# Performance work log

Hardware: AMD Instinct MI355X
Metric: run time of the kernel (lower is better)

## Reference

```python
import jax, jax.numpy as jnp
import numpy as np

B = 4096
T = 66            # total_char_ids = 51 + 8 + 6 + 1
EMB = 128
ITEM_EMB = 64     # emb_dim // 2
NUM_ITEMS = 287
ITEMS_IN_GAME = 70  # 7 * 10
N_SCREEN = 24
N_MINI = 40
CONT = 32


def _unique_ids(key, batch, n):
    keys = jax.random.split(key, batch)
    return jax.vmap(lambda k: jax.random.permutation(k, T)[:n])(keys).astype(jnp.int32)


def setup_inputs() -> dict:
    key = jax.random.key(0)
    ks = jax.random.split(key, 16)
    inp = {
        "continuous_f": jax.random.normal(ks[0], (B, CONT), jnp.float32),
        "screen_feats": jax.random.uniform(ks[1], (B, N_SCREEN, 4), jnp.float32),
        "minimap_feats": jax.random.uniform(ks[2], (B, N_MINI, 2), jnp.float32),
        "char_emb": jax.random.normal(ks[3], (T, EMB), jnp.float32) * 0.02,
        "item_emb": jax.random.normal(ks[4], (NUM_ITEMS, ITEM_EMB), jnp.float32) * 0.02,
        "Ws1": jax.random.normal(ks[5], (EMB + 4, EMB), jnp.float32) * 0.05,
        "bs1": jnp.zeros((EMB,), jnp.float32),
        "Ws2": jax.random.normal(ks[6], (EMB, EMB), jnp.float32) * 0.05,
        "bs2": jnp.zeros((EMB,), jnp.float32),
        "Wm1": jax.random.normal(ks[7], (EMB + 2, EMB), jnp.float32) * 0.05,
        "bm1": jnp.zeros((EMB,), jnp.float32),
        "Wm2": jax.random.normal(ks[8], (EMB, EMB), jnp.float32) * 0.05,
        "bm2": jnp.zeros((EMB,), jnp.float32),
        "screen_ids": _unique_ids(ks[9], B, N_SCREEN),
        "minimap_ids": _unique_ids(ks[10], B, N_MINI),
        "items": jax.random.randint(ks[11], (B, ITEMS_IN_GAME), 0, NUM_ITEMS, jnp.int32),
    }
    return inp


def reference(continuous_f, screen_feats, minimap_feats, char_emb, item_emb,
              Ws1, bs1, Ws2, bs2, Wm1, bm1, Wm2, bm2,
              screen_ids, minimap_ids, items):
    b = continuous_f.shape[0]
    rows = jnp.arange(b)[:, None]

    # scatter detections by char id into fixed [T, .] buffers (vectorized over batch)
    scr = jnp.zeros((b, T, 4), screen_feats.dtype).at[rows, screen_ids].set(screen_feats)
    mini = jnp.zeros((b, T, 2), minimap_feats.dtype).at[rows, minimap_ids].set(minimap_feats)

    # item embedding lookup -> [b, 70*64]
    item_flat = item_emb[items].reshape(b, -1)

    base = jnp.broadcast_to(char_emb, (b, T, EMB))  # all char ids embedded

    def mlp(x, W1, b1, W2, b2):
        h = jax.nn.relu(jnp.einsum('btf,fh->bth', x, W1) + b1)
        return jnp.einsum('bth,hk->btk', h, W2) + b2

    screen_out = mlp(jnp.concatenate([base, scr], axis=-1), Ws1, bs1, Ws2, bs2)
    mini_out = mlp(jnp.concatenate([base, mini], axis=-1), Wm1, bm1, Wm2, bm2)

    obs = jnp.concatenate(
        [continuous_f, screen_out.reshape(b, -1), mini_out.reshape(b, -1), item_flat],
        axis=-1)  # [b, 32 + 66*128 + 66*128 + 70*64] = [b, 21408]
    return obs
```

## Files before the change

### kernel.cpp

```cpp
#include <hip/hip_runtime.h>
#include <stdint.h>

#define BDIM 256
#define T_   66
#define EMB  128
#define NS   24
#define NM   40
#define NI   70
#define CONT 32
#define OUTW 21408

typedef __attribute__((ext_vector_type(4))) float f32x4;
typedef __attribute__((ext_vector_type(8))) unsigned short u16x8;
typedef __attribute__((ext_vector_type(8))) __bf16 bf16x8;

static __device__ __forceinline__ unsigned short f2bf(float x) {
  union { float f; unsigned u; } v; v.f = x;
  unsigned r = (v.u + 0x7FFFu + ((v.u >> 16) & 1u)) >> 16;
  return (unsigned short)r;
}

static __device__ __forceinline__ f32x4 mfma16(u16x8 a, u16x8 b, f32x4 c) {
  return __builtin_amdgcn_mfma_f32_16x16x32_bf16(
      __builtin_bit_cast(bf16x8, a), __builtin_bit_cast(bf16x8, b), c, 0, 0, 0);
}

__global__ __launch_bounds__(BDIM) void precomp(
    const float* __restrict__ char_emb,
    const float* __restrict__ Ws1, const float* __restrict__ bs1,
    const float* __restrict__ Ws2, const float* __restrict__ bs2,
    const float* __restrict__ Wm1, const float* __restrict__ bm1,
    const float* __restrict__ Wm2, const float* __restrict__ bm2,
    float* __restrict__ base_h_s, float* __restrict__ base_h_m,
    float* __restrict__ base_out_s, float* __restrict__ base_out_m,
    unsigned short* __restrict__ w2s_swz, unsigned short* __restrict__ w2m_swz) {
  const int bb = blockIdx.x, tid = threadIdx.x;
  if (bb < 132) {
    const int mlp = bb / T_, t = bb % T_;
    const float* W1 = mlp ? Wm1 : Ws1;
    const float* W2 = mlp ? Wm2 : Ws2;
    const float* b1 = mlp ? bm1 : bs1;
    const float* b2 = mlp ? bm2 : bs2;
    float* bh = mlp ? base_h_m : base_h_s;
    float* bo = mlp ? base_out_m : base_out_s;
    __shared__ float h[EMB];
    if (tid < EMB) {
      float acc = b1[tid];
      for (int f = 0; f < EMB; ++f) acc += char_emb[t * EMB + f] * W1[f * EMB + tid];
      bh[t * EMB + tid] = acc;
      h[tid] = fmaxf(acc, 0.f);
    }
    __syncthreads();
    if (tid < EMB) {
      float acc = b2[tid];
      for (int i = 0; i < EMB; ++i) acc += h[i] * W2[i * EMB + tid];
      bo[t * EMB + tid] = acc;
    }
  } else {
    const int mlp = bb - 132;
    const float* W2 = mlp ? Wm2 : Ws2;
    unsigned short* dst = mlp ? w2m_swz : w2s_swz;
    for (int idx = tid; idx < 8 * 4 * 64 * 8; idx += BDIM) {
      const int e = idx & 7, lane = (idx >> 3) & 63, kk = (idx >> 9) & 3, n = idx >> 11;
      const int k = kk * 32 + (lane >> 4) * 8 + e;
      const int col = n * 16 + (lane & 15);
      dst[idx] = f2bf(W2[k * EMB + col]);
    }
  }
}

__global__ __launch_bounds__(BDIM) void fused(
    const float* __restrict__ contf,
    const float* __restrict__ sfeat,
    const float* __restrict__ mfeat,
    const float* __restrict__ item_emb,
    const float* __restrict__ Ws1,
    const float* __restrict__ bs2,
    const float* __restrict__ Wm1,
    const float* __restrict__ bm2,
    const int* __restrict__ sids,
    const int* __restrict__ mids,
    const int* __restrict__ items,
    const float* __restrict__ base_h_s, const float* __restrict__ base_h_m,
    const float* __restrict__ base_out_s, const float* __restrict__ base_out_m,
    const unsigned short* __restrict__ w2s_swz, const unsigned short* __restrict__ w2m_swz,
    float* __restrict__ out) {
  const int b = blockIdx.x, tid = threadIdx.x;

  __shared__ int s_map[T_], m_map[T_];
  __shared__ int s_id[NS], m_id[NM], s_item[NI];
  __shared__ float s_f[NS * 4], m_f[NM * 2];
  __shared__ u16x8 h_frag[5 * 4 * 64];
  __shared__ float det_out[48 * 132];

  if (tid < T_) { s_map[tid] = -1; m_map[tid] = -1; }
  if (tid < NS) s_id[tid] = sids[b * NS + tid];
  if (tid < NM) m_id[tid] = mids[b * NM + tid];
  if (tid < NI) s_item[tid] = items[b * NI + tid];
  if (tid < NS * 4) s_f[tid] = sfeat[b * NS * 4 + tid];
  if (tid < NM * 2) m_f[tid] = mfeat[b * NM * 2 + tid];
  __syncthreads();
  if (tid < NS) s_map[s_id[tid]] = tid;
  if (tid < NM) m_map[m_id[tid]] = tid;

  for (int u = tid; u < 5 * 4 * 64; u += BDIM) {
    const int lane = u & 63, kk = (u >> 6) & 3, tile = u >> 8;
    const int g = lane >> 4, r = lane & 15;
    const int k0 = kk * 32 + g * 8;
    const bool scr = tile < 2;
    const int j = scr ? tile * 16 + r : (tile - 2) * 16 + r;
    const int nd = scr ? NS : NM;
    float v[8];
    if (j < nd) {
      const int t = scr ? s_id[j] : m_id[j];
      const float* bh = (scr ? base_h_s : base_h_m) + t * EMB + k0;
#pragma unroll
      for (int e = 0; e < 8; ++e) v[e] = bh[e];
      if (scr) {
        const float* fp = &s_f[j * 4];
#pragma unroll
        for (int c = 0; c < 4; ++c) {
          const float fc = fp[c];
          const float* w = Ws1 + (128 + c) * EMB + k0;
#pragma unroll
          for (int e = 0; e < 8; ++e) v[e] += fc * w[e];
        }
      } else {
        const float* fp = &m_f[j * 2];
#pragma unroll
        for (int c = 0; c < 2; ++c) {
          const float fc = fp[c];
          const float* w = Wm1 + (128 + c) * EMB + k0;
#pragma unroll
          for (int e = 0; e < 8; ++e) v[e] += fc * w[e];
        }
      }
#pragma unroll
      for (int e = 0; e < 8; ++e) v[e] = fmaxf(v[e], 0.f);
    } else {
#pragma unroll
      for (int e = 0; e < 8; ++e) v[e] = 0.f;
    }
    u16x8 pk;
#pragma unroll
    for (int e = 0; e < 8; ++e) pk[e] = f2bf(v[e]);
    h_frag[u] = pk;
  }
  __syncthreads();

  {
    f32x4* ob = reinterpret_cast<f32x4*>(out + (size_t)b * OUTW);
    const f32x4* cb = reinterpret_cast<const f32x4*>(contf + (size_t)b * CONT);
    for (int u = tid; u < 8 + NI * 16; u += BDIM) {
      if (u < 8) {
        __builtin_nontemporal_store(cb[u], &ob[u]);
      } else {
        const int v2 = u - 8, j = v2 >> 4, q = v2 & 15;
        const int it = s_item[j];
        const f32x4 src = reinterpret_cast<const f32x4*>(item_emb + it * 64)[q];
        __builtin_nontemporal_store(src, reinterpret_cast<f32x4*>(
            out + (size_t)b * OUTW + (CONT + 2 * T_ * EMB) + j * 64) + q);
      }
    }
  }

  const int w = tid >> 6, lane = tid & 63;
  const int g = lane >> 4, r = lane & 15;
  const int n0 = w * 2;

  {
    u16x8 bS[2][4];
    float biasS[2];
#pragma unroll
    for (int n = 0; n < 2; ++n) {
      biasS[n] = bs2[(n0 + n) * 16 + r];
#pragma unroll
      for (int kk = 0; kk < 4; ++kk)
        bS[n][kk] = reinterpret_cast<const u16x8*>(w2s_swz)[((n0 + n) * 4 + kk) * 64 + lane];
    }
#pragma unroll
    for (int m = 0; m < 2; ++m) {
#pragma unroll
      for (int n = 0; n < 2; ++n) {
        f32x4 acc = {0.f, 0.f, 0.f, 0.f};
#pragma unroll
        for (int kk = 0; kk < 4; ++kk)
          acc = mfma16(h_frag[(m * 4 + kk) * 64 + lane], bS[n][kk], acc);
        const int col = (n0 + n) * 16 + r;
#pragma unroll
        for (int q = 0; q < 4; ++q)
          det_out[(m * 16 + g * 4 + q) * 132 + col] = acc[q] + biasS[n];
      }
    }
  }
  __syncthreads();

  {
    float* outp = out + (size_t)b * OUTW + CONT;
    for (int u = tid; u < T_ * 32; u += BDIM) {
      const int t = u >> 5, q = u & 31;
      const int d = s_map[t];
      f32x4 v;
      if (d >= 0) v = *reinterpret_cast<const f32x4*>(&det_out[d * 132 + q * 4]);
      else        v = reinterpret_cast<const f32x4*>(base_out_s + t * EMB)[q];
      __builtin_nontemporal_store(v, reinterpret_cast<f32x4*>(outp + t * EMB) + q);
    }
  }
  __syncthreads();

  {
    u16x8 bM[2][4];
    float biasM[2];
#pragma unroll
    for (int n = 0; n < 2; ++n) {
      biasM[n] = bm2[(n0 + n) * 16 + r];
#pragma unroll
      for (int kk = 0; kk < 4; ++kk)
        bM[n][kk] = reinterpret_cast<const u16x8*>(w2m_swz)[((n0 + n) * 4 + kk) * 64 + lane];
    }
#pragma unroll
    for (int m = 0; m < 3; ++m) {
#pragma unroll
      for (int n = 0; n < 2; ++n) {
        f32x4 acc = {0.f, 0.f, 0.f, 0.f};
#pragma unroll
        for (int kk = 0; kk < 4; ++kk)
          acc = mfma16(h_frag[((m + 2) * 4 + kk) * 64 + lane], bM[n][kk], acc);
        const int col = (n0 + n) * 16 + r;
#pragma unroll
        for (int q = 0; q < 4; ++q)
          det_out[(m * 16 + g * 4 + q) * 132 + col] = acc[q] + biasM[n];
      }
    }
  }
  __syncthreads();

  {
    float* outp = out + (size_t)b * OUTW + CONT + T_ * EMB;
    for (int u = tid; u < T_ * 32; u += BDIM) {
      const int t = u >> 5, q = u & 31;
      const int d = m_map[t];
      f32x4 v;
      if (d >= 0) v = *reinterpret_cast<const f32x4*>(&det_out[d * 132 + q * 4]);
      else        v = reinterpret_cast<const f32x4*>(base_out_m + t * EMB)[q];
      __builtin_nontemporal_store(v, reinterpret_cast<f32x4*>(outp + t * EMB) + q);
    }
  }
}

extern "C" void kernel_launch(void* const* d_in, const int* in_sizes, int n_in,
                              void* d_out, int out_size, void* d_ws, size_t ws_size,
                              hipStream_t stream) {
  const float* contf    = (const float*)d_in[0];
  const float* sfeat    = (const float*)d_in[1];
  const float* mfeat    = (const float*)d_in[2];
  const float* char_emb = (const float*)d_in[3];
  const float* item_emb = (const float*)d_in[4];
  const float* Ws1 = (const float*)d_in[5];
  const float* bs1 = (const float*)d_in[6];
  const float* Ws2 = (const float*)d_in[7];
  const float* bs2 = (const float*)d_in[8];
  const float* Wm1 = (const float*)d_in[9];
  const float* bm1 = (const float*)d_in[10];
  const float* Wm2 = (const float*)d_in[11];
  const float* bm2 = (const float*)d_in[12];
  const int* sids  = (const int*)d_in[13];
  const int* mids  = (const int*)d_in[14];
  const int* items = (const int*)d_in[15];
  float* out = (float*)d_out;

  const int B = in_sizes[0] / CONT;

  char* ws = (char*)d_ws;
  float* base_h_s   = (float*)(ws + 0);
  float* base_h_m   = (float*)(ws + 33792);
  float* base_out_s = (float*)(ws + 67584);
  float* base_out_m = (float*)(ws + 101376);
  unsigned short* w2s = (unsigned short*)(ws + 135168);
  unsigned short* w2m = (unsigned short*)(ws + 167936);

  precomp<<<134, BDIM, 0, stream>>>(char_emb, Ws1, bs1, Ws2, bs2, Wm1, bm1, Wm2, bm2,
                                    base_h_s, base_h_m, base_out_s, base_out_m, w2s, w2m);
  fused<<<B, BDIM, 0, stream>>>(contf, sfeat, mfeat, item_emb, Ws1, bs2, Wm1, bm2,
                                sids, mids, items,
                                base_h_s, base_h_m, base_out_s, base_out_m, w2s, w2m, out);
}
```

Baseline: 98.12 us.

## Scatter MFMA results straight to global, drop LDS staging, widen blocks to 512

The fused kernel now writes each detection's MLP output directly from the MFMA accumulators to its scattered output row, and writes base rows only for char ids with no detection. This removes the det_out LDS buffer and the extra barriers between the screen and minimap phases. Block size doubles to 512 so each wave owns one 16-column N tile, and the bias is folded into the accumulator init. The precompute kernel splits the K dimension across four thread groups and covers both MLPs in one block. The price is scalar scattered global stores, narrower than the previous 16-byte vector writes, and lower occupancy per CU from the larger blocks.

Measured after the change: 99.00 us. About the same (+0.9%).

```diff
diff --git a/kernel.cpp b/kernel.cpp
--- a/kernel.cpp
+++ b/kernel.cpp
@@ -1,7 +1,8 @@
 #include <hip/hip_runtime.h>
 #include <stdint.h>
 
-#define BDIM 256
+#define BDIM 512
+#define PDIM 512
 #define T_   66
 #define EMB  128
 #define NS   24
@@ -25,7 +26,7 @@
       __builtin_bit_cast(bf16x8, a), __builtin_bit_cast(bf16x8, b), c, 0, 0, 0);
 }
 
-__global__ __launch_bounds__(BDIM) void precomp(
+__global__ __launch_bounds__(PDIM) void precomp(
     const float* __restrict__ char_emb,
     const float* __restrict__ Ws1, const float* __restrict__ bs1,
     const float* __restrict__ Ws2, const float* __restrict__ bs2,
@@ -35,32 +36,45 @@
     float* __restrict__ base_out_s, float* __restrict__ base_out_m,
     unsigned short* __restrict__ w2s_swz, unsigned short* __restrict__ w2m_swz) {
   const int bb = blockIdx.x, tid = threadIdx.x;
-  if (bb < 132) {
-    const int mlp = bb / T_, t = bb % T_;
+  if (bb < T_) {
+    const int t = bb;
+    const int quarter = tid >> 7;
+    const int col = tid & 127;
+    const int mlp = quarter & 1;
+    const int kh = quarter >> 1;
     const float* W1 = mlp ? Wm1 : Ws1;
     const float* W2 = mlp ? Wm2 : Ws2;
     const float* b1 = mlp ? bm1 : bs1;
     const float* b2 = mlp ? bm2 : bs2;
     float* bh = mlp ? base_h_m : base_h_s;
     float* bo = mlp ? base_out_m : base_out_s;
-    __shared__ float h[EMB];
-    if (tid < EMB) {
-      float acc = b1[tid];
-      for (int f = 0; f < EMB; ++f) acc += char_emb[t * EMB + f] * W1[f * EMB + tid];
-      bh[t * EMB + tid] = acc;
-      h[tid] = fmaxf(acc, 0.f);
-    }
+    __shared__ float part[4][EMB];
+    __shared__ float h[2][EMB];
+    float acc = 0.f;
+#pragma unroll 8
+    for (int f = kh * 64; f < kh * 64 + 64; ++f)
+      acc += char_emb[t * EMB + f] * W1[f * EMB + col];
+    part[quarter][col] = acc;
     __syncthreads();
-    if (tid < EMB) {
-      float acc = b2[tid];
-      for (int i = 0; i < EMB; ++i) acc += h[i] * W2[i * EMB + tid];
-      bo[t * EMB + tid] = acc;
-    }
+    if (tid < 256) {
+      const float v = b1[col] + part[mlp][col] + part[2 + mlp][col];
+      bh[t * EMB + col] = v;
+      h[mlp][col] = fmaxf(v, 0.f);
+    }
+    __syncthreads();
+    float acc2 = 0.f;
+#pragma unroll 8
+    for (int i = kh * 64; i < kh * 64 + 64; ++i)
+      acc2 += h[mlp][i] * W2[i * EMB + col];
+    part[quarter][col] = acc2;
+    __syncthreads();
+    if (tid < 256)
+      bo[t * EMB + col] = b2[col] + part[mlp][col] + part[2 + mlp][col];
   } else {
-    const int mlp = bb - 132;
+    const int mlp = bb - T_;
     const float* W2 = mlp ? Wm2 : Ws2;
     unsigned short* dst = mlp ? w2m_swz : w2s_swz;
-    for (int idx = tid; idx < 8 * 4 * 64 * 8; idx += BDIM) {
+    for (int idx = tid; idx < 8 * 4 * 64 * 8; idx += PDIM) {
       const int e = idx & 7, lane = (idx >> 3) & 63, kk = (idx >> 9) & 3, n = idx >> 11;
       const int k = kk * 32 + (lane >> 4) * 8 + e;
       const int col = n * 16 + (lane & 15);
@@ -91,7 +105,6 @@
   __shared__ int s_id[NS], m_id[NM], s_item[NI];
   __shared__ float s_f[NS * 4], m_f[NM * 2];
   __shared__ u16x8 h_frag[5 * 4 * 64];
-  __shared__ float det_out[48 * 132];
 
   if (tid < T_) { s_map[tid] = -1; m_map[tid] = -1; }
   if (tid < NS) s_id[tid] = sids[b * NS + tid];
@@ -100,9 +113,9 @@
   if (tid < NS * 4) s_f[tid] = sfeat[b * NS * 4 + tid];
   if (tid < NM * 2) m_f[tid] = mfeat[b * NM * 2 + tid];
   __syncthreads();
+
   if (tid < NS) s_map[s_id[tid]] = tid;
   if (tid < NM) m_map[m_id[tid]] = tid;
-
   for (int u = tid; u < 5 * 4 * 64; u += BDIM) {
     const int lane = u & 63, kk = (u >> 6) & 3, tile = u >> 8;
     const int g = lane >> 4, r = lane & 15;
@@ -121,18 +134,18 @@
 #pragma unroll
         for (int c = 0; c < 4; ++c) {
           const float fc = fp[c];
-          const float* w = Ws1 + (128 + c) * EMB + k0;
-#pragma unroll
-          for (int e = 0; e < 8; ++e) v[e] += fc * w[e];
+          const float* wp = Ws1 + (128 + c) * EMB + k0;
+#pragma unroll
+          for (int e = 0; e < 8; ++e) v[e] += fc * wp[e];
         }
       } else {
         const float* fp = &m_f[j * 2];
 #pragma unroll
         for (int c = 0; c < 2; ++c) {
           const float fc = fp[c];
-          const float* w = Wm1 + (128 + c) * EMB + k0;
-#pragma unroll
-          for (int e = 0; e < 8; ++e) v[e] += fc * w[e];
+          const float* wp = Wm1 + (128 + c) * EMB + k0;
+#pragma unroll
+          for (int e = 0; e < 8; ++e) v[e] += fc * wp[e];
         }
       }
 #pragma unroll
@@ -147,10 +160,72 @@
     h_frag[u] = pk;
   }
   __syncthreads();
+
+  const int lane = tid & 63, w = tid >> 6;
+  const int g = lane >> 4, r = lane & 15;
+  const int n = w;
+  float* outS = out + (size_t)b * OUTW + CONT;
+  float* outM = outS + T_ * EMB;
+
+  u16x8 bS[4], bM[4];
+#pragma unroll
+  for (int kk = 0; kk < 4; ++kk) {
+    bS[kk] = reinterpret_cast<const u16x8*>(w2s_swz)[(n * 4 + kk) * 64 + lane];
+    bM[kk] = reinterpret_cast<const u16x8*>(w2m_swz)[(n * 4 + kk) * 64 + lane];
+  }
+  const float biasS = bs2[n * 16 + r];
+  const float biasM = bm2[n * 16 + r];
+
+#pragma unroll
+  for (int m = 0; m < 2; ++m) {
+    f32x4 acc = {biasS, biasS, biasS, biasS};
+#pragma unroll
+    for (int kk = 0; kk < 4; ++kk)
+      acc = mfma16(h_frag[(m * 4 + kk) * 64 + lane], bS[kk], acc);
+#pragma unroll
+    for (int q = 0; q < 4; ++q) {
+      const int rd = m * 16 + g * 4 + q;
+      if (rd < NS) {
+        const int t = s_id[rd];
+        __builtin_nontemporal_store(acc[q], outS + t * EMB + n * 16 + r);
+      }
+    }
+  }
+#pragma unroll
+  for (int m = 0; m < 3; ++m) {
+    f32x4 acc = {biasM, biasM, biasM, biasM};
+#pragma unroll
+    for (int kk = 0; kk < 4; ++kk)
+      acc = mfma16(h_frag[((m + 2) * 4 + kk) * 64 + lane], bM[kk], acc);
+#pragma unroll
+    for (int q = 0; q < 4; ++q) {
+      const int rd = m * 16 + g * 4 + q;
+      if (rd < NM) {
+        const int t = m_id[rd];
+        __builtin_nontemporal_store(acc[q], outM + t * EMB + n * 16 + r);
+      }
+    }
+  }
+
+  for (int u = tid; u < T_ * 32; u += BDIM) {
+    const int t = u >> 5, q = u & 31;
+    if (s_map[t] < 0) {
+      const f32x4 v = reinterpret_cast<const f32x4*>(base_out_s + t * EMB)[q];
+      __builtin_nontemporal_store(v, reinterpret_cast<f32x4*>(outS + t * EMB) + q);
+    }
+  }
+  for (int u = tid; u < T_ * 32; u += BDIM) {
+    const int t = u >> 5, q = u & 31;
+    if (m_map[t] < 0) {
+      const f32x4 v = reinterpret_cast<const f32x4*>(base_out_m + t * EMB)[q];
+      __builtin_nontemporal_store(v, reinterpret_cast<f32x4*>(outM + t * EMB) + q);
+    }
+  }
 
   {
     f32x4* ob = reinterpret_cast<f32x4*>(out + (size_t)b * OUTW);
     const f32x4* cb = reinterpret_cast<const f32x4*>(contf + (size_t)b * CONT);
+    float* outI = out + (size_t)b * OUTW + (CONT + 2 * T_ * EMB);
     for (int u = tid; u < 8 + NI * 16; u += BDIM) {
       if (u < 8) {
         __builtin_nontemporal_store(cb[u], &ob[u]);
@@ -158,92 +233,8 @@
         const int v2 = u - 8, j = v2 >> 4, q = v2 & 15;
         const int it = s_item[j];
         const f32x4 src = reinterpret_cast<const f32x4*>(item_emb + it * 64)[q];
-        __builtin_nontemporal_store(src, reinterpret_cast<f32x4*>(
-            out + (size_t)b * OUTW + (CONT + 2 * T_ * EMB) + j * 64) + q);
-      }
-    }
-  }
-
-  const int w = tid >> 6, lane = tid & 63;
-  const int g = lane >> 4, r = lane & 15;
-  const int n0 = w * 2;
-
-  {
-    u16x8 bS[2][4];
-    float biasS[2];
-#pragma unroll
-    for (int n = 0; n < 2; ++n) {
-      biasS[n] = bs2[(n0 + n) * 16 + r];
-#pragma unroll
-      for (int kk = 0; kk < 4; ++kk)
-        bS[n][kk] = reinterpret_cast<const u16x8*>(w2s_swz)[((n0 + n) * 4 + kk) * 64 + lane];
-    }
-#pragma unroll
-    for (int m = 0; m < 2; ++m) {
-#pragma unroll
-      for (int n = 0; n < 2; ++n) {
-        f32x4 acc = {0.f, 0.f, 0.f, 0.f};
-#pragma unroll
-        for (int kk = 0; kk < 4; ++kk)
-          acc = mfma16(h_frag[(m * 4 + kk) * 64 + lane], bS[n][kk], acc);
-        const int col = (n0 + n) * 16 + r;
-#pragma unroll
-        for (int q = 0; q < 4; ++q)
-          det_out[(m * 16 + g * 4 + q) * 132 + col] = acc[q] + biasS[n];
-      }
-    }
-  }
-  __syncthreads();
-
-  {
-    float* outp = out + (size_t)b * OUTW + CONT;
-    for (int u = tid; u < T_ * 32; u += BDIM) {
-      const int t = u >> 5, q = u & 31;
-      const int d = s_map[t];
-      f32x4 v;
-      if (d >= 0) v = *reinterpret_cast<const f32x4*>(&det_out[d * 132 + q * 4]);
-      else        v = reinterpret_cast<const f32x4*>(base_out_s + t * EMB)[q];
-      __builtin_nontemporal_store(v, reinterpret_cast<f32x4*>(outp + t * EMB) + q);
-    }
-  }
-  __syncthreads();
-
-  {
-    u16x8 bM[2][4];
-    float biasM[2];
-#pragma unroll
-    for (int n = 0; n < 2; ++n) {
-      biasM[n] = bm2[(n0 + n) * 16 + r];
-#pragma unroll
-      for (int kk = 0; kk < 4; ++kk)
-        bM[n][kk] = reinterpret_cast<const u16x8*>(w2m_swz)[((n0 + n) * 4 + kk) * 64 + lane];
-    }
-#pragma unroll
-    for (int m = 0; m < 3; ++m) {
-#pragma unroll
-      for (int n = 0; n < 2; ++n) {
-        f32x4 acc = {0.f, 0.f, 0.f, 0.f};
-#pragma unroll
-        for (int kk = 0; kk < 4; ++kk)
-          acc = mfma16(h_frag[((m + 2) * 4 + kk) * 64 + lane], bM[n][kk], acc);
-        const int col = (n0 + n) * 16 + r;
-#pragma unroll
-        for (int q = 0; q < 4; ++q)
-          det_out[(m * 16 + g * 4 + q) * 132 + col] = acc[q] + biasM[n];
-      }
-    }
-  }
-  __syncthreads();
-
-  {
-    float* outp = out + (size_t)b * OUTW + CONT + T_ * EMB;
-    for (int u = tid; u < T_ * 32; u += BDIM) {
-      const int t = u >> 5, q = u & 31;
-      const int d = m_map[t];
-      f32x4 v;
-      if (d >= 0) v = *reinterpret_cast<const f32x4*>(&det_out[d * 132 + q * 4]);
-      else        v = reinterpret_cast<const f32x4*>(base_out_m + t * EMB)[q];
-      __builtin_nontemporal_store(v, reinterpret_cast<f32x4*>(outp + t * EMB) + q);
+        __builtin_nontemporal_store(src, reinterpret_cast<f32x4*>(outI + j * 64) + q);
+      }
     }
   }
 }
@@ -279,8 +270,8 @@
   unsigned short* w2s = (unsigned short*)(ws + 135168);
   unsigned short* w2m = (unsigned short*)(ws + 167936);
 
-  precomp<<<134, BDIM, 0, stream>>>(char_emb, Ws1, bs1, Ws2, bs2, Wm1, bm1, Wm2, bm2,
-                                    base_h_s, base_h_m, base_out_s, base_out_m, w2s, w2m);
+  precomp<<<T_ + 2, PDIM, 0, stream>>>(char_emb, Ws1, bs1, Ws2, bs2, Wm1, bm1, Wm2, bm2,
+                                       base_h_s, base_h_m, base_out_s, base_out_m, w2s, w2m);
   fused<<<B, BDIM, 0, stream>>>(contf, sfeat, mfeat, item_emb, Ws1, bs2, Wm1, bm2,
                                 sids, mids, items,
                                 base_h_s, base_h_m, base_out_s, base_out_m, w2s, w2m, out);
```
